# Optimization experiments

Measured on AMD Instinct MI355X. Metric: run time of the kernel, lower is better.

## Reference

```python
import jax, jax.numpy as jnp
import numpy as np

B, N, T = 32, 256, 256
W, H, EMB = 32, 128, 64          # window_size, tgcn_hidden_dim, gsl_embed_dim
K, ALPHA, NC, E = 3, 1.0, 16, 8192  # gsl_avg_steps, gsl_alpha, num_classes, static edges
GCN_IN = W + H                    # GSL gconv in_channels
THRESH = 1e-8


def setup_inputs():
    ks = jax.random.split(jax.random.key(0), 24)
    rng = np.random.default_rng(0)
    src = rng.integers(0, N, size=E)
    tgt = (src + 1 + rng.integers(0, N - 1, size=E)) % N  # no self-loops (PyG adds them)
    edge_index = jnp.asarray(np.stack([src, tgt]), dtype=jnp.int32)

    def p(k, shape):
        return jax.random.normal(k, shape, jnp.float32) * (shape[0] ** -0.5)

    z = lambda n: jnp.zeros((n,), jnp.float32)
    return {
        "x": jax.random.normal(ks[0], (B, N, T), jnp.float32),
        "static_edge_index": edge_index,
        "static_edge_weight": jax.random.uniform(ks[1], (E,), jnp.float32),
        "Wg": p(ks[2], (GCN_IN, EMB)), "bg": z(EMB),
        "W1": p(ks[3], (EMB, EMB)), "b1": z(EMB),
        "W2": p(ks[4], (EMB, EMB)), "b2": z(EMB),
        "Wz": p(ks[5], (W, H)), "bz": z(H),
        "Wr": p(ks[6], (W, H)), "br": z(H),
        "Wh": p(ks[7], (W, H)), "bh": z(H),
        "Wlz": p(ks[8], (2 * H, H)), "blz": z(H),
        "Wlr": p(ks[9], (2 * H, H)), "blr": z(H),
        "Wlh": p(ks[10], (2 * H, H)), "blh": z(H),
        "Wc": p(ks[11], (H * N, NC)), "bc": z(NC),
    }


def _forward(x, edge_index, edge_weight, Wg, bg, W1, b1, W2, b2,
             Wz, bz, Wr, br, Wh, bh, Wlz, blz, Wlr, blr, Wlh, blh, Wc, bc):
    dt = x.dtype
    eye = jnp.eye(N, dtype=dt)

    # Static graph: dense adjacency + self loops, symmetric GCN normalization.
    A = jnp.zeros((N, N), dt).at[edge_index[0], edge_index[1]].add(edge_weight) + eye
    deg = A.sum(0)  # in-degree at targets (col sums)
    di = jnp.where(deg > 0, jax.lax.rsqrt(deg), 0.0)
    S = di[:, None] * A * di[None, :]  # S[r,c]; out[c] = sum_r S[r,c] x[r]

    # windowing: v[t,b,n,:] = x[b,n,t*W:(t+1)*W]
    v = x.reshape(B, N, T // W, W).transpose(2, 0, 1, 3)  # [nw,B,N,W]

    def gcn_norm_b(Ad):  # Ad [B,N,N], zero diagonal guaranteed
        Ah = Ad + eye
        d = Ah.sum(-2)
        q = jnp.where(d > 0, jax.lax.rsqrt(d), 0.0)
        return q[:, :, None] * Ah * q[:, None, :]

    def step(carry, vt):
        h, hist, cnt = carry  # h [B,N,H], hist [K,B,N,N]
        It = jnp.concatenate([vt, h], -1)                   # [B,N,W+H]
        df = jnp.einsum('rc,brf->bcf', S, It @ Wg) + bg     # static GCNConv
        de1 = jnp.tanh(ALPHA * (df @ W1 + b1))
        de2 = jnp.tanh(ALPHA * (df @ W2 + b2))
        M = jnp.einsum('bne,bme->bnm', de1, de2)            # de1 @ de2^T
        Et = jax.nn.relu(jnp.tanh(ALPHA * (M - M.transpose(0, 2, 1))))
        hist = jnp.concatenate([hist[1:], Et[None]], 0)     # deque(maxlen=K)
        cnt = jnp.minimum(cnt + 1, K)
        Mt = hist.sum(0) / cnt.astype(dt)
        An = gcn_norm_b(jnp.where(Mt > THRESH, Mt, jnp.zeros((), dt)))

        def conv(Wk, bk):  # dynamic GCNConv, block-diag == per-batch dense
            return jnp.einsum('brc,brf->bcf', An, vt @ Wk) + bk

        Z = jax.nn.sigmoid(jnp.concatenate([conv(Wz, bz), h], -1) @ Wlz + blz)
        R = jax.nn.sigmoid(jnp.concatenate([conv(Wr, br), h], -1) @ Wlr + blr)
        Ht = jnp.tanh(jnp.concatenate([conv(Wh, bh), h * R], -1) @ Wlh + blh)
        h = Z * h + (1.0 - Z) * Ht
        return (h, hist, cnt), None

    h0 = jnp.zeros((B, N, H), dt)
    hist0 = jnp.zeros((K, B, N, N), dt)
    (h, _, _), _ = jax.lax.scan(step, (h0, hist0, jnp.int32(0)), v)
    return h.reshape(B, N * H) @ Wc + bc  # [B, NC]


def reference(x, static_edge_index, static_edge_weight, Wg, bg, W1, b1, W2, b2,
              Wz, bz, Wr, br, Wh, bh, Wlz, blz, Wlr, blr, Wlh, blh, Wc, bc):
    return _forward(x, static_edge_index, static_edge_weight, Wg, bg, W1, b1, W2, b2,
                    Wz, bz, Wr, br, Wh, bh, Wlz, blz, Wlr, blr, Wlh, blh, Wc, bc)
```

## Files before the change

kernel.cpp:

```cpp
#include <hip/hip_runtime.h>
#include <hip/hip_bf16.h>
#include <math.h>

#define BB  32
#define NN  256
#define TT  256
#define WW  32
#define HH  128
#define EMBD 64
#define NCLS 16
#define NE  8192

__device__ __forceinline__ float bf(const __hip_bfloat16* p, int i) {
    return __bfloat162float(p[i]);
}
__device__ __forceinline__ float ld3(const void* p, int i, int m) {
    if (m == 2) return (float)((const double*)p)[i];
    if (m == 1) return ((const float*)p)[i];
    return __bfloat162float(((const __hip_bfloat16*)p)[i]);
}
__device__ __forceinline__ float r16(float x) {
    return __bfloat162float(__float2bfloat16(x));
}
__device__ __forceinline__ float tanh_s(float x) {
    x = fminf(20.0f, fmaxf(-20.0f, x));
    return tanhf(x);
}
__device__ __forceinline__ float sig_s(float x) {
    x = fminf(30.0f, fmaxf(-30.0f, x));
    return 1.0f / (1.0f + expf(-x));
}


__global__ __launch_bounds__(64) void k_sentinel(float* out, float v) {
    int i = blockIdx.x * 64 + threadIdx.x;
    if (i < BB * NCLS) out[i] = v;
}

__global__ __launch_bounds__(256) void k_probe_all(
        const void* x, const void* ew, const void* Wg, const void* W1, const void* W2,
        const void* Wz, const void* Wr, const void* Wh, const void* Wlz, const void* Wlr,
        const void* Wlh, const void* Wc, int* insB, int* insF) {
    int sec = blockIdx.x >> 2, sub = blockIdx.x & 3;
    const void* p; int nB, idx;
    switch (sec) {
        case 0:  p = x;   nB = 32768; idx = 0;  break;
        case 1:  p = ew;  nB = 8192;  idx = 2;  break;
        case 2:  p = Wg;  nB = 10240; idx = 3;  break;
        case 3:  p = W1;  nB = 4096;  idx = 5;  break;
        case 4:  p = W2;  nB = 4096;  idx = 7;  break;
        case 5:  p = Wz;  nB = 4096;  idx = 9;  break;
        case 6:  p = Wr;  nB = 4096;  idx = 11; break;
        case 7:  p = Wh;  nB = 4096;  idx = 13; break;
        case 8:  p = Wlz; nB = 32768; idx = 15; break;
        case 9:  p = Wlr; nB = 32768; idx = 17; break;
        case 10: p = Wlh; nB = 32768; idx = 19; break;
        default: p = Wc;  nB = 32768; idx = 21; break;
    }
    int nF = nB >> 2;
    const __hip_bfloat16* pb = (const __hip_bfloat16*)p;
    const float* pf = (const float*)p;
    int start = sub * 256 + threadIdx.x;
    for (int i = start; i < nB; i += 1024) {
        float v = __bfloat162float(pb[i]);
        if (!(fabsf(v) < 64.0f)) { insB[idx] = 1; break; }
    }
    for (int i = start; i < nF; i += 1024) {
        float v = pf[i];
        if (!(fabsf(v) < 1e4f)) { insF[idx] = 1; break; }
    }
}

__global__ void k_resolve(const int* insB, const int* insF, int* modes) {
    int i = threadIdx.x;
    if (i < 32 && i != 1)
        modes[i] = insB[i] ? (insF[i] ? 2 : 1) : 0;
}

__global__ __launch_bounds__(64) void k_detect_ei(const int* ei, int* modes) {
    if (threadIdx.x == 0 && blockIdx.x == 0) {
        bool allz = true;
        for (int k = 1; k < 64; k += 2) if (ei[k] != 0) allz = false;
        modes[1] = allz ? 1 : 0;
    }
}

__global__ __launch_bounds__(256) void k_cvtall(const void* Wg, const void* W1, const void* W2,
                                                const void* Wz, const void* Wr, const void* Wh,
                                                const void* Wlz, const void* Wlr, const void* Wlh,
                                                const void* Wc, const int* modes, float* dst) {
    int i = blockIdx.x * 256 + threadIdx.x;
    if (i >= 665600) return;
    float v;
    if      (i < 10240)  v = ld3(Wg,  i,          modes[3]);
    else if (i < 14336)  v = ld3(W1,  i - 10240,  modes[5]);
    else if (i < 18432)  v = ld3(W2,  i - 14336,  modes[7]);
    else if (i < 22528)  v = ld3(Wz,  i - 18432,  modes[9]);
    else if (i < 26624)  v = ld3(Wr,  i - 22528,  modes[11]);
    else if (i < 30720)  v = ld3(Wh,  i - 26624,  modes[13]);
    else if (i < 63488)  v = ld3(Wlz, i - 30720,  modes[15]);
    else if (i < 96256)  v = ld3(Wlr, i - 63488,  modes[17]);
    else if (i < 129024) v = ld3(Wlh, i - 96256,  modes[19]);
    else if (i < 653312) v = ld3(Wc,  i - 129024, modes[21]);
    else {
        int j = i - 653312, w = j / 384, rem = j - w * 384;
        int g = rem >> 7, f = rem & 127;
        const void* Wk = (g == 0) ? Wz : ((g == 1) ? Wr : Wh);
        int mk = (g == 0) ? modes[9] : ((g == 1) ? modes[11] : modes[13]);
        v = ld3(Wk, w * 128 + f, mk);
    }
    dst[i] = v;
}

__global__ __launch_bounds__(256) void k_fuse(const float* Wzf, const float* Wrf, const float* Whf,
                                              const float* Wlzf, const float* Wlrf, const float* Wlhf,
                                              const __hip_bfloat16* bz, const __hip_bfloat16* br,
                                              const __hip_bfloat16* bh,
                                              const __hip_bfloat16* blz, const __hip_bfloat16* blr,
                                              const __hip_bfloat16* blh,
                                              float* Wf, float* bfv) {
    int g = blockIdx.y;
    const float* Wcv = (g == 0) ? Wzf : ((g == 1) ? Wrf : Whf);
    const float* Wl  = (g == 0) ? Wlzf : ((g == 1) ? Wlrf : Wlhf);
    const __hip_bfloat16* bcv = (g == 0) ? bz : ((g == 1) ? br : bh);
    const __hip_bfloat16* blv = (g == 0) ? blz : ((g == 1) ? blr : blh);
    int idx = blockIdx.x * 256 + threadIdx.x;
    if (idx >= 160 * 128) return;
    int k = idx >> 7, f = idx & 127;
    float v;
    if (k < 32) {
        float acc = 0.f;
        for (int m = 0; m < 128; m++) acc += Wcv[k * 128 + m] * Wl[m * 128 + f];
        v = acc;
    } else {
        v = Wl[(k + 96) * 128 + f];
    }
    Wf[((size_t)g * 160 + k) * 128 + f] = v;
    if (idx < 128) {
        float acc = __bfloat162float(blv[idx]);
        for (int m = 0; m < 128; m++) acc += __bfloat162float(bcv[m]) * Wl[m * 128 + idx];
        bfv[g * 128 + idx] = acc;
    }
}


__global__ __launch_bounds__(256) void k_scatter(const int* ei, const void* ew, float* A,
                                                 const int* modes) {
    int e = blockIdx.x * 256 + threadIdx.x;
    if (e < NE) {
        int s, t;
        if (modes[1]) { s = ei[2 * e]; t = ei[2 * (NE + e)]; }
        else          { s = ei[e];     t = ei[NE + e]; }
        float w = r16(ld3(ew, e, modes[2]));
        if ((unsigned)s < NN && (unsigned)t < NN)
            atomicAdd(&A[s * NN + t], w);
    }
    if (blockIdx.x == 0) atomicAdd(&A[threadIdx.x * NN + threadIdx.x], 1.0f);
}

__global__ __launch_bounds__(256) void k_roundA(float* A) {
    int i = blockIdx.x * 256 + threadIdx.x;
    A[i] = r16(A[i]);
}

__global__ __launch_bounds__(256) void k_di(const float* A, float* di) {
    int wave = threadIdx.x >> 6, lane = threadIdx.x & 63;
    int c = blockIdx.x * 4 + wave;
    float s = 0.f;
    for (int r = lane; r < NN; r += 64) s += A[r * NN + c];
    for (int o = 32; o > 0; o >>= 1) s += __shfl_down(s, o, 64);
    if (lane == 0) {
        float deg = r16(s);
        di[c] = (deg > 0.f) ? r16(1.0f / sqrtf(deg)) : 0.0f;
    }
}

__global__ __launch_bounds__(256) void k_St(const float* A, const float* di, float* St) {
    int idx = blockIdx.x * 256 + threadIdx.x;
    int c = idx >> 8, r = idx & 255;
    St[idx] = r16(r16(di[r] * A[r * NN + c]) * di[c]);
}


__global__ __launch_bounds__(256) void k1_itwg4(const void* x, const float* h,
                                                const float* Wgf, float* Y,
                                                int t, const int* modes) {
    __shared__ float vt[4][32];
    __shared__ float hr[4][128];
    int b = blockIdx.y, n0 = blockIdx.x * 4;
    int tid = threadIdx.x;
    int nd = tid >> 6, f = tid & 63;
    if (f < WW) vt[nd][f] = ld3(x, (b * NN + n0 + nd) * TT + t * WW + f, modes[0]);
    size_t hb = (size_t)(b * NN + n0 + nd) * HH;
    hr[nd][f] = h[hb + f];
    hr[nd][f + 64] = h[hb + f + 64];
    __syncthreads();
    float acc = 0.f;
    for (int k = 0; k < WW; k++)  acc += vt[nd][k] * Wgf[k * EMBD + f];
    for (int k = 0; k < HH; k++)  acc += hr[nd][k] * Wgf[(WW + k) * EMBD + f];
    if (t == 0 && modes[0] == 0 && modes[3] == 0) acc = r16(acc);
    Y[(size_t)(b * NN + n0 + nd) * EMBD + f] = acc;
}

__global__ __launch_bounds__(256) void k23g(const float* St, const float* Y,
                                            const __hip_bfloat16* bg,
                                            const float* W1f, const float* W2f,
                                            const __hip_bfloat16* b1, const __hip_bfloat16* b2,
                                            float* de1, float* de2, float* qsum,
                                            int t, const int* modes) {
    __shared__ float As[32][36];
    __shared__ float Bs[32][68];
    __shared__ float dfT[64][36];
    int b = blockIdx.y, c0 = blockIdx.x * 32;
    int tid = threadIdx.x;
    if (blockIdx.x == 0) qsum[b * NN + tid] = 0.f;
    int tm = tid >> 4, tn = tid & 15;
    int am = tid & 31, ak0 = (tid >> 5) * 4;
    int bk = tid >> 3, bn0 = (tid & 7) * 8;
    const float* Yb = Y + (size_t)b * (NN * EMBD);
    float acc[2][4] = {};
    for (int kb = 0; kb < 256; kb += 32) {
        float4 a0 = *(const float4*)(St + (size_t)(c0 + am) * 256 + kb + ak0);
        float av4[4] = {a0.x, a0.y, a0.z, a0.w};
        int rot = (tid >> 5) & 3;
#pragma unroll
        for (int jj = 0; jj < 4; jj++) { int j = (jj + rot) & 3; As[ak0 + j][am] = av4[j]; }
        const float* bp = Yb + (size_t)(kb + bk) * 64 + bn0;
        *(float4*)&Bs[bk][bn0]     = *(const float4*)bp;
        *(float4*)&Bs[bk][bn0 + 4] = *(const float4*)(bp + 4);
        __syncthreads();
#pragma unroll
        for (int kk = 0; kk < 32; kk++) {
            float2 av = *(const float2*)&As[kk][tm * 2];
            float4 bv = *(const float4*)&Bs[kk][tn * 4];
            float aa[2] = {av.x, av.y};
            float bb[4] = {bv.x, bv.y, bv.z, bv.w};
#pragma unroll
            for (int i = 0; i < 2; i++)
#pragma unroll
                for (int j = 0; j < 4; j++) acc[i][j] += aa[i] * bb[j];
        }
        __syncthreads();
    }
    bool rnd = (t == 0 && modes[0] == 0 && modes[3] == 0);
#pragma unroll
    for (int i = 0; i < 2; i++)
#pragma unroll
        for (int j = 0; j < 4; j++) {
            int f = tn * 4 + j;
            float v = (rnd ? r16(acc[i][j]) : acc[i][j]) + bf(bg, f);
            dfT[f][tm * 2 + i] = v;
        }
    __syncthreads();
    float a1acc[2][4] = {};
    for (int kb2 = 0; kb2 < 64; kb2 += 32) {
        const float* bp = W1f + (size_t)(kb2 + bk) * 64 + bn0;
        *(float4*)&Bs[bk][bn0]     = *(const float4*)bp;
        *(float4*)&Bs[bk][bn0 + 4] = *(const float4*)(bp + 4);
        __syncthreads();
#pragma unroll
        for (int kk = 0; kk < 32; kk++) {
            float2 av = *(const float2*)&dfT[kb2 + kk][tm * 2];
            float4 bv = *(const float4*)&Bs[kk][tn * 4];
            float aa[2] = {av.x, av.y};
            float bb[4] = {bv.x, bv.y, bv.z, bv.w};
#pragma unroll
            for (int i = 0; i < 2; i++)
#pragma unroll
                for (int j = 0; j < 4; j++) a1acc[i][j] += aa[i] * bb[j];
        }
        __syncthreads();
    }
#pragma unroll
    for (int i = 0; i < 2; i++) {
        int row = b * NN + c0 + tm * 2 + i;
        float4 o;
        o.x = tanh_s(a1acc[i][0] + bf(b1, tn * 4 + 0));
        o.y = tanh_s(a1acc[i][1] + bf(b1, tn * 4 + 1));
        o.z = tanh_s(a1acc[i][2] + bf(b1, tn * 4 + 2));
        o.w = tanh_s(a1acc[i][3] + bf(b1, tn * 4 + 3));
        *(float4*)&de1[(size_t)row * 64 + tn * 4] = o;
    }
    float a2acc[2][4] = {};
    for (int kb2 = 0; kb2 < 64; kb2 += 32) {
        const float* bp = W2f + (size_t)(kb2 + bk) * 64 + bn0;
        *(float4*)&Bs[bk][bn0]     = *(const float4*)bp;
        *(float4*)&Bs[bk][bn0 + 4] = *(const float4*)(bp + 4);
        __syncthreads();
#pragma unroll
        for (int kk = 0; kk < 32; kk++) {
            float2 av = *(const float2*)&dfT[kb2 + kk][tm * 2];
            float4 bv = *(const float4*)&Bs[kk][tn * 4];
            float aa[2] = {av.x, av.y};
            float bb[4] = {bv.x, bv.y, bv.z, bv.w};
#pragma unroll
            for (int i = 0; i < 2; i++)
#pragma unroll
                for (int j = 0; j < 4; j++) a2acc[i][j] += aa[i] * bb[j];
        }
        __syncthreads();
    }
#pragma unroll
    for (int i = 0; i < 2; i++) {
        int row = b * NN + c0 + tm * 2 + i;
        float4 o;
        o.x = tanh_s(a2acc[i][0] + bf(b2, tn * 4 + 0));
        o.y = tanh_s(a2acc[i][1] + bf(b2, tn * 4 + 1));
        o.z = tanh_s(a2acc[i][2] + bf(b2, tn * 4 + 2));
        o.w = tanh_s(a2acc[i][3] + bf(b2, tn * 4 + 3));
        *(float4*)&de2[(size_t)row * 64 + tn * 4] = o;
    }
}

__global__ __launch_bounds__(256) void k45(const float* de1, const float* de2,
                                           float* hist, float* AhT, float* qsum,
                                           int slabW, int slabR, float inv_cnt) {
    __shared__ float As[32][68];
    __shared__ float Bs[32][68];
    __shared__ float m2b[64][65];
    __shared__ float qpart[64];
    int b = blockIdx.z, r0 = blockIdx.x * 64, c0 = blockIdx.y * 64;
    int tid = threadIdx.x;
    if (tid < 64) qpart[tid] = 0.f;
    int tn = tid & 15, tm = tid >> 4;
    int am = tid >> 2, ak0 = (tid & 3) * 8;
    int rot = (tid & 3) * 2;
    const float* d1 = de1 + (size_t)b * (NN * EMBD);
    const float* d2 = de2 + (size_t)b * (NN * EMBD);
    float acc2[4][4] = {};
    for (int kb = 0; kb < 64; kb += 32) {
        const float* ap = d1 + (size_t)(c0 + am) * 64 + kb + ak0;
        float4 a0 = *(const float4*)ap;
        float4 a1 = *(const float4*)(ap + 4);
        float av8[8] = {a0.x, a0.y, a0.z, a0.w, a1.x, a1.y, a1.z, a1.w};
#pragma unroll
        for (int jj = 0; jj < 8; jj++) { int j = (jj + rot) & 7; As[ak0 + j][am] = av8[j]; }
        const float* bp = d2 + (size_t)(r0 + am) * 64 + kb + ak0;
        float4 b0 = *(const float4*)bp;
        float4 b1v = *(const float4*)(bp + 4);
        float bv8[8] = {b0.x, b0.y, b0.z, b0.w, b1v.x, b1v.y, b1v.z, b1v.w};
#pragma unroll
        for (int jj = 0; jj < 8; jj++) { int j = (jj + rot) & 7; Bs[ak0 + j][am] = bv8[j]; }
        __syncthreads();
#pragma unroll
        for (int kk = 0; kk < 32; kk++) {
            float4 av = *(const float4*)&As[kk][tm * 4];
            float4 bv = *(const float4*)&Bs[kk][tn * 4];
            float aa[4] = {av.x, av.y, av.z, av.w};
            float bb[4] = {bv.x, bv.y, bv.z, bv.w};
#pragma unroll
            for (int i = 0; i < 4; i++)
#pragma unroll
                for (int j = 0; j < 4; j++) acc2[i][j] += aa[i] * bb[j];
        }
        __syncthreads();
    }
#pragma unroll
    for (int i = 0; i < 4; i++)
#pragma unroll
        for (int j = 0; j < 4; j++) m2b[tm * 4 + i][tn * 4 + j] = acc2[i][j];
    float acc1[4][4] = {};
    for (int kb = 0; kb < 64; kb += 32) {
        const float* ap = d1 + (size_t)(r0 + am) * 64 + kb + ak0;
        float4 a0 = *(const float4*)ap;
        float4 a1 = *(const float4*)(ap + 4);
        float av8[8] = {a0.x, a0.y, a0.z, a0.w, a1.x, a1.y, a1.z, a1.w};
#pragma unroll
        for (int jj = 0; jj < 8; jj++) { int j = (jj + rot) & 7; As[ak0 + j][am] = av8[j]; }
        const float* bp = d2 + (size_t)(c0 + am) * 64 + kb + ak0;
        float4 b0 = *(const float4*)bp;
        float4 b1v = *(const float4*)(bp + 4);
        float bv8[8] = {b0.x, b0.y, b0.z, b0.w, b1v.x, b1v.y, b1v.z, b1v.w};
#pragma unroll
        for (int jj = 0; jj < 8; jj++) { int j = (jj + rot) & 7; Bs[ak0 + j][am] = bv8[j]; }
        __syncthreads();
#pragma unroll
        for (int kk = 0; kk < 32; kk++) {
            float4 av = *(const float4*)&As[kk][tm * 4];
            float4 bv = *(const float4*)&Bs[kk][tn * 4];
            float aa[4] = {av.x, av.y, av.z, av.w};
            float bb[4] = {bv.x, bv.y, bv.z, bv.w};
#pragma unroll
            for (int i = 0; i < 4; i++)
#pragma unroll
                for (int j = 0; j < 4; j++) acc1[i][j] += aa[i] * bb[j];
        }
        __syncthreads();
    }
    size_t NB = (size_t)BB * NN * NN;
    float* hsW = hist + (size_t)slabW * NB;
    const float* hsR = hist + (size_t)slabR * NB;
    float ad[4][4];
#pragma unroll
    for (int i = 0; i < 4; i++) {
        int r = r0 + tm * 4 + i;
        size_t o = ((size_t)(b * NN + r)) * NN + c0 + tn * 4;
        float4 e2v = *(const float4*)&hsW[o];
        float4 e1v = *(const float4*)&hsR[o];
        float e2a[4] = {e2v.x, e2v.y, e2v.z, e2v.w};
        float e1a[4] = {e1v.x, e1v.y, e1v.z, e1v.w};
        float4 ew4;
        float eo[4];
#pragma unroll
        for (int j = 0; j < 4; j++) {
            int c = c0 + tn * 4 + j;
            float e = tanh_s(acc1[i][j] - m2b[tn * 4 + j][tm * 4 + i]);
            e = e > 0.f ? e : 0.f;
            eo[j] = e;
            float mt = (e + e1a[j] + e2a[j]) * inv_cnt;
            float adv = (mt > 1e-8f) ? mt : 0.f;
            if (r == c) adv += 1.f;
            ad[i][j] = adv;
        }
        ew4.x = eo[0]; ew4.y = eo[1]; ew4.z = eo[2]; ew4.w = eo[3];
        *(float4*)&hsW[o] = ew4;
    }
#pragma unroll
    for (int j = 0; j < 4; j++) {
        float cs = ad[0][j] + ad[1][j] + ad[2][j] + ad[3][j];
        atomicAdd(&qpart[tn * 4 + j], cs);
    }
    __syncthreads();
#pragma unroll
    for (int i = 0; i < 4; i++)
#pragma unroll
        for (int j = 0; j < 4; j++) m2b[tn * 4 + j][tm * 4 + i] = ad[i][j];
    __syncthreads();
#pragma unroll
    for (int kk = 0; kk < 4; kk++) {
        int e = tid + kk * 256;
        int cl = e >> 4, q4 = e & 15;
        float4 o;
        o.x = m2b[cl][q4 * 4 + 0]; o.y = m2b[cl][q4 * 4 + 1];
        o.z = m2b[cl][q4 * 4 + 2]; o.w = m2b[cl][q4 * 4 + 3];
        *(float4*)&AhT[((size_t)(b * NN + c0 + cl)) * NN + r0 + q4 * 4] = o;
    }
    if (tid < 64) atomicAdd(&qsum[b * NN + c0 + tid], qpart[tid]);
}

__global__ __launch_bounds__(256) void k8a(const float* AhT, const void* x, const float* qsum,
                                           float* G, int t, const int* modes) {
    __shared__ float As[32][36];
    __shared__ float Bs[32][36];
    int b = blockIdx.y, c0 = blockIdx.x * 32;
    int tid = threadIdx.x;
    int tm = tid >> 3, tn = tid & 7;
    int am = tid & 31, ak0 = (tid >> 5) * 8;
    int rB = tid >> 3, w0 = (tid & 7) * 4;
    int m0 = modes[0];
    const float* Ab = AhT + (size_t)b * (NN * NN);
    float acc[4] = {0, 0, 0, 0};
    for (int kb = 0; kb < 256; kb += 32) {
        const float* ap = Ab + (size_t)(c0 + am) * 256 + kb + ak0;
        float4 a0 = *(const float4*)ap;
        float4 a1 = *(const float4*)(ap + 4);
        float av8[8] = {a0.x, a0.y, a0.z, a0.w, a1.x, a1.y, a1.z, a1.w};
#pragma unroll
        for (int j = 0; j < 8; j++) As[ak0 + j][am] = av8[j];
        int r = kb + rB;
        float qr = 1.0f / sqrtf(fmaxf(qsum[b * NN + r], 1e-12f));
        int xbase = (b * NN + r) * TT + t * WW + w0;
        float pv[4];
#pragma unroll
        for (int i = 0; i < 4; i++) pv[i] = qr * ld3(x, xbase + i, m0);
        int rot = rB & 3;
#pragma unroll
        for (int i = 0; i < 4; i++) {
            int j = (i + rot) & 3;
            Bs[rB][w0 + j] = pv[j];
        }
        __syncthreads();
#pragma unroll
        for (int kk = 0; kk < 32; kk++) {
            float a = As[kk][tm];
            float4 bv = *(const float4*)&Bs[kk][tn * 4];
            acc[0] += a * bv.x; acc[1] += a * bv.y;
            acc[2] += a * bv.z; acc[3] += a * bv.w;
        }
        __syncthreads();
    }
    int c = c0 + tm;
    float qc = 1.0f / sqrtf(fmaxf(qsum[b * NN + c], 1e-12f));
    float4 o = make_float4(qc * acc[0], qc * acc[1], qc * acc[2], qc * acc[3]);
    *(float4*)&G[((size_t)(b * NN + c)) * 32 + tn * 4] = o;
}

__global__ __launch_bounds__(256) void kZRH16(const float* G, float* h,
                                              const float* Wf, const float* bfv,
                                              const float* Wgf, const void* x, float* Y,
                                              int t, const int* modes) {
    __shared__ float As[160 * 18];
    __shared__ float Bs[2 * 32 * 128];
    int r0 = blockIdx.x * 16;
    int tid = threadIdx.x;
    int m0 = modes[0];
    if (tid < 128) {
        int r = tid >> 3, c4 = (tid & 7) * 4;
        float4 gv = *(const float4*)&G[(size_t)(r0 + r) * 32 + c4];
        As[(c4 + 0) * 18 + r] = gv.x;
        As[(c4 + 1) * 18 + r] = gv.y;
        As[(c4 + 2) * 18 + r] = gv.z;
        As[(c4 + 3) * 18 + r] = gv.w;
    }
#pragma unroll
    for (int u = 0; u < 2; u++) {
        int e = tid * 2 + u;
        int r = e >> 5, c4 = (e & 31) * 4;
        float4 hv = *(const float4*)&h[(size_t)(r0 + r) * 128 + c4];
        As[(32 + c4 + 0) * 18 + r] = hv.x;
        As[(32 + c4 + 1) * 18 + r] = hv.y;
        As[(32 + c4 + 2) * 18 + r] = hv.z;
        As[(32 + c4 + 3) * 18 + r] = hv.w;
    }
    int rg = tid >> 5, cg = tid & 31;
    float zv[2][4], rv[2][4];
    {
        const float* W0 = Wf;
        const float* W1 = Wf + (size_t)(160 * 128);
        float accZ[2][4] = {};
        float accR[2][4] = {};
        for (int kb = 0; kb < 160; kb += 32) {
#pragma unroll
            for (int u = 0; u < 4; u++) {
                int e = tid + u * 256;
                int kk = e >> 5, c4 = (e & 31) * 4;
                *(float4*)&Bs[kk * 128 + c4]        = *(const float4*)&W0[(size_t)(kb + kk) * 128 + c4];
                *(float4*)&Bs[4096 + kk * 128 + c4] = *(const float4*)&W1[(size_t)(kb + kk) * 128 + c4];
            }
            __syncthreads();
#pragma unroll 4
            for (int kk = 0; kk < 32; kk++) {
                float2 av = *(const float2*)&As[(kb + kk) * 18 + rg * 2];
                float4 b0 = *(const float4*)&Bs[kk * 128 + cg * 4];
                float4 b1 = *(const float4*)&Bs[4096 + kk * 128 + cg * 4];
                accZ[0][0] += av.x * b0.x; accZ[0][1] += av.x * b0.y;
                accZ[0][2] += av.x * b0.z; accZ[0][3] += av.x * b0.w;
                accZ[1][0] += av.y * b0.x; accZ[1][1] += av.y * b0.y;
                accZ[1][2] += av.y * b0.z; accZ[1][3] += av.y * b0.w;
                accR[0][0] += av.x * b1.x; accR[0][1] += av.x * b1.y;
                accR[0][2] += av.x * b1.z; accR[0][3] += av.x * b1.w;
                accR[1][0] += av.y * b1.x; accR[1][1] += av.y * b1.y;
                accR[1][2] += av.y * b1.z; accR[1][3] += av.y * b1.w;
            }
            __syncthreads();
        }
#pragma unroll
        for (int i = 0; i < 2; i++)
#pragma unroll
            for (int j = 0; j < 4; j++) {
                zv[i][j] = sig_s(accZ[i][j] + bfv[cg * 4 + j]);
                rv[i][j] = sig_s(accR[i][j] + bfv[128 + cg * 4 + j]);
            }
    }
#pragma unroll
    for (int i = 0; i < 2; i++)
#pragma unroll
        for (int j = 0; j < 4; j++) {
            int slot = (32 + cg * 4 + j) * 18 + rg * 2 + i;
            As[slot] = As[slot] * rv[i][j];
        }
    __syncthreads();
    float acc[2][4] = {};
    {
        const float* Wgp = Wf + (size_t)2 * (160 * 128);
        for (int kb = 0; kb < 160; kb += 32) {
#pragma unroll
            for (int u = 0; u < 4; u++) {
                int e = tid + u * 256;
                int kk = e >> 5, c4 = (e & 31) * 4;
                *(float4*)&Bs[kk * 128 + c4] = *(const float4*)&Wgp[(size_t)(kb + kk) * 128 + c4];
            }
            __syncthreads();
#pragma unroll 4
            for (int kk = 0; kk < 32; kk++) {
                float2 av = *(const float2*)&As[(kb + kk) * 18 + rg * 2];
                float4 bv = *(const float4*)&Bs[kk * 128 + cg * 4];
                acc[0][0] += av.x * bv.x; acc[0][1] += av.x * bv.y;
                acc[0][2] += av.x * bv.z; acc[0][3] += av.x * bv.w;
                acc[1][0] += av.y * bv.x; acc[1][1] += av.y * bv.y;
                acc[1][2] += av.y * bv.z; acc[1][3] += av.y * bv.w;
            }
            __syncthreads();
        }
    }
#pragma unroll
    for (int i = 0; i < 2; i++) {
        int row = r0 + rg * 2 + i;
        size_t o = (size_t)row * 128 + cg * 4;
        float4 hv = *(const float4*)&h[o];
        float4 r;
        r.x = zv[i][0] * hv.x + (1.0f - zv[i][0]) * tanh_s(acc[i][0] + bfv[256 + cg * 4 + 0]);
        r.y = zv[i][1] * hv.y + (1.0f - zv[i][1]) * tanh_s(acc[i][1] + bfv[256 + cg * 4 + 1]);
        r.z = zv[i][2] * hv.z + (1.0f - zv[i][2]) * tanh_s(acc[i][2] + bfv[256 + cg * 4 + 2]);
        r.w = zv[i][3] * hv.w + (1.0f - zv[i][3]) * tanh_s(acc[i][3] + bfv[256 + cg * 4 + 3]);
        *(float4*)&h[o] = r;
        As[(32 + cg * 4 + 0) * 18 + rg * 2 + i] = r.x;
        As[(32 + cg * 4 + 1) * 18 + rg * 2 + i] = r.y;
        As[(32 + cg * 4 + 2) * 18 + rg * 2 + i] = r.z;
        As[(32 + cg * 4 + 3) * 18 + rg * 2 + i] = r.w;
    }
    if (t < 7) {
#pragma unroll
        for (int u = 0; u < 2; u++) {
            int e = tid * 2 + u;
            int r = e >> 5, w = e & 31;
            As[w * 18 + r] = ld3(x, (r0 + r) * TT + (t + 1) * WW + w, m0);
        }
        __syncthreads();
        int yr = tid >> 4, yc4 = (tid & 15) * 4;
        float yacc[4] = {0.f, 0.f, 0.f, 0.f};
        for (int kb = 0; kb < 160; kb += 32) {
#pragma unroll
            for (int u = 0; u < 2; u++) {
                int e = tid * 2 + u;
                int kk = e >> 4, c4 = (e & 15) * 4;
                *(float4*)&Bs[kk * 64 + c4] = *(const float4*)&Wgf[(size_t)(kb + kk) * 64 + c4];
            }
            __syncthreads();
#pragma unroll 4
            for (int kk = 0; kk < 32; kk++) {
                float a = As[(kb + kk) * 18 + yr];
                float4 bv = *(const float4*)&Bs[kk * 64 + yc4];
                yacc[0] += a * bv.x; yacc[1] += a * bv.y;
                yacc[2] += a * bv.z; yacc[3] += a * bv.w;
            }
            __syncthreads();
        }
        *(float4*)&Y[(size_t)(r0 + yr) * 64 + yc4] =
            make_float4(yacc[0], yacc[1], yacc[2], yacc[3]);
    }
}

__global__ __launch_bounds__(256) void k10a(const float* h, const float* Wcf, float* partial) {
    __shared__ float red[16][17];
    int chunk = blockIdx.x, b = blockIdx.y;
    int c = threadIdx.x & 15, isub = threadIdx.x >> 4;
    const float* hb = h + (size_t)b * (NN * HH);
    int i0 = chunk * 2048;
    float acc = 0.f;
    for (int s = 0; s < 128; s++) {
        int i = i0 + isub + 16 * s;
        acc += hb[i] * Wcf[(size_t)i * NCLS + c];
    }
    red[isub][c] = acc;
    __syncthreads();
    for (int st = 8; st > 0; st >>= 1) {
        if (isub < st) red[isub][c] += red[isub + st][c];
        __syncthreads();
    }
    if (isub == 0) partial[((size_t)(b * NCLS + c)) * 16 + chunk] = red[0][c];
}

__global__ __launch_bounds__(512) void k10b(const float* partial, const __hip_bfloat16* bcb,
                                            float* out) {
    int tid = threadIdx.x;
    if (tid < BB * NCLS) {
        int c = tid & 15;
        float s = 0.f;
        for (int k = 0; k < 16; k++) s += partial[(size_t)tid * 16 + k];
        out[tid] = s + bf(bcb, c);
    }
}


extern "C" void kernel_launch(void* const* d_in, const int* in_sizes, int n_in,
                              void* d_out, int out_size, void* d_ws, size_t ws_size,
                              hipStream_t stream) {
    float* out = (float*)d_out;

    static const int exp_sizes[23] = {2097152, 16384, 8192, 10240, 64, 4096, 64, 4096, 64,
                                      4096, 128, 4096, 128, 4096, 128, 32768, 128, 32768, 128,
                                      32768, 128, 524288, 16};
    if (n_in != 23) { k_sentinel<<<8, 64, 0, stream>>>(out, 4444.0f); return; }
    for (int i = 0; i < 23; i++) {
        if (in_sizes[i] != exp_sizes[i]) {
            k_sentinel<<<8, 64, 0, stream>>>(out, (float)(4000 + i));
            return;
        }
    }

    const void* x   = d_in[0];
    const int*  ei  = (const int*)d_in[1];
    const void* ew  = d_in[2];
    const void* Wg  = d_in[3];
    const __hip_bfloat16* bg  = (const __hip_bfloat16*)d_in[4];
    const void* W1  = d_in[5];
    const __hip_bfloat16* b1  = (const __hip_bfloat16*)d_in[6];
    const void* W2  = d_in[7];
    const __hip_bfloat16* b2  = (const __hip_bfloat16*)d_in[8];
    const void* Wz  = d_in[9];
    const __hip_bfloat16* bz  = (const __hip_bfloat16*)d_in[10];
    const void* Wr  = d_in[11];
    const __hip_bfloat16* br  = (const __hip_bfloat16*)d_in[12];
    const void* Wh  = d_in[13];
    const __hip_bfloat16* bh  = (const __hip_bfloat16*)d_in[14];
    const void* Wlz = d_in[15];
    const __hip_bfloat16* blz = (const __hip_bfloat16*)d_in[16];
    const void* Wlr = d_in[17];
    const __hip_bfloat16* blr = (const __hip_bfloat16*)d_in[18];
    const void* Wlh = d_in[19];
    const __hip_bfloat16* blh = (const __hip_bfloat16*)d_in[20];
    const void* Wc  = d_in[21];
    const __hip_bfloat16* bcb = (const __hip_bfloat16*)d_in[22];

    float* ws = (float*)d_ws;
    const size_t off_A    = 0;
    const size_t off_hist = off_A + 65536;
    const size_t off_h    = off_hist + 2u * 2097152;
    const size_t off_flag = off_h + 1048576;
    const size_t off_mode = off_flag + 16;
    const size_t off_insB = off_mode + 32;
    const size_t off_insF = off_insB + 32;
    const size_t zero_end = off_insF + 32;
    const size_t off_St   = zero_end;
    const size_t off_di   = off_St + 65536;
    const size_t off_q    = off_di + 256;
    const size_t off_AhT  = off_q + 8192;
    const size_t off_Yp   = off_AhT + 2097152;
    const size_t off_C    = off_Yp + 3145728;
    const size_t off_wts  = off_C + 3145728;
    const size_t need_bytes = (off_wts + 665600u) * sizeof(float);

    if (ws_size < need_bytes) {
        k_sentinel<<<8, 64, 0, stream>>>(out, (float)ws_size);
        return;
    }

    float* A    = ws + off_A;
    float* hist = ws + off_hist;
    float* h    = ws + off_h;
    int*   modes= (int*)(ws + off_mode);
    int*   insB = (int*)(ws + off_insB);
    int*   insF = (int*)(ws + off_insF);
    float* St   = ws + off_St;
    float* di   = ws + off_di;
    float* qsum = ws + off_q;
    float* AhT  = ws + off_AhT;
    float* wts  = ws + off_wts;
    float* Y    = ws + off_Yp;
    float* de1  = ws + off_Yp + 1048576;
    float* de2  = ws + off_Yp + 1572864;
    float* G    = ws + off_Yp + 2097152;
    float* Wf   = ws + off_C;
    float* bfv  = ws + off_C + 61440;
    float* partial = qsum;

    float* Wgf  = wts;
    float* W1f  = wts + 10240;
    float* W2f  = wts + 14336;
    float* Wzf  = wts + 18432;
    float* Wrf  = wts + 22528;
    float* Whf  = wts + 26624;
    float* Wlzf = wts + 30720;
    float* Wlrf = wts + 63488;
    float* Wlhf = wts + 96256;
    float* Wcf  = wts + 129024;

    hipMemsetAsync(ws, 0, zero_end * sizeof(float), stream);

    k_probe_all<<<48, 256, 0, stream>>>(x, ew, Wg, W1, W2, Wz, Wr, Wh, Wlz, Wlr, Wlh, Wc,
                                        insB, insF);
    k_resolve<<<1, 32, 0, stream>>>(insB, insF, modes);
    k_detect_ei<<<1, 64, 0, stream>>>(ei, modes);
    k_cvtall<<<2600, 256, 0, stream>>>(Wg, W1, W2, Wz, Wr, Wh, Wlz, Wlr, Wlh, Wc, modes, wts);
    k_fuse<<<dim3(80, 3), 256, 0, stream>>>(Wzf, Wrf, Whf, Wlzf, Wlrf, Wlhf,
                                            bz, br, bh, blz, blr, blh, Wf, bfv);

    k_scatter<<<NE / 256, 256, 0, stream>>>(ei, ew, A, modes);
    k_roundA<<<NN * NN / 256, 256, 0, stream>>>(A);
    k_di<<<NN / 4, 256, 0, stream>>>(A, di);
    k_St<<<NN * NN / 256, 256, 0, stream>>>(A, di, St);

    for (int t = 0; t < 8; t++) {
        if (t == 0)
            k1_itwg4<<<dim3(NN / 4, BB), 256, 0, stream>>>(x, h, Wgf, Y, 0, modes);
        k23g<<<dim3(8, BB), 256, 0, stream>>>(St, Y, bg, W1f, W2f, b1, b2,
                                              de1, de2, qsum, t, modes);
        float inv_cnt = 1.0f / (float)((t + 1 < 3) ? (t + 1) : 3);
        k45<<<dim3(4, 4, BB), 256, 0, stream>>>(de1, de2, hist, AhT, qsum,
                                                t & 1, (t + 1) & 1, inv_cnt);
        k8a<<<dim3(NN / 32, BB), 256, 0, stream>>>(AhT, x, qsum, G, t, modes);
        kZRH16<<<NN * BB / 16, 256, 0, stream>>>(G, h, Wf, bfv, Wgf, x, Y, t, modes);
    }

    k10a<<<dim3(16, BB), 256, 0, stream>>>(h, Wcf, partial);
    k10b<<<1, 512, 0, stream>>>(partial, bcb, out);
}
```

Before: 874.2 us.

## Fuse normalized adjacency-times-window GEMM into the ZRH gate kernel

Removes the separate k8a kernel that computed G = q_c * AhT * (q_r * x_window) and instead computes each 16-row block of G inside kZRH16, writing it straight into the shared-memory A tile. This drops one launch per timestep and the global round-trip through the G buffer. In exchange, each of the 512 blocks reloads the full 256x32 normalized window slice for its batch (16x redundant x reads) and runs a scalar inner product loop, and shared memory use grows.

```diff
diff --git a/kernel.cpp b/kernel.cpp
--- a/kernel.cpp
+++ b/kernel.cpp
@@ -438,70 +438,17 @@
     if (tid < 64) atomicAdd(&qsum[b * NN + c0 + tid], qpart[tid]);
 }
 
-__global__ __launch_bounds__(256) void k8a(const float* AhT, const void* x, const float* qsum,
-                                           float* G, int t, const int* modes) {
-    __shared__ float As[32][36];
-    __shared__ float Bs[32][36];
-    int b = blockIdx.y, c0 = blockIdx.x * 32;
-    int tid = threadIdx.x;
-    int tm = tid >> 3, tn = tid & 7;
-    int am = tid & 31, ak0 = (tid >> 5) * 8;
-    int rB = tid >> 3, w0 = (tid & 7) * 4;
-    int m0 = modes[0];
-    const float* Ab = AhT + (size_t)b * (NN * NN);
-    float acc[4] = {0, 0, 0, 0};
-    for (int kb = 0; kb < 256; kb += 32) {
-        const float* ap = Ab + (size_t)(c0 + am) * 256 + kb + ak0;
-        float4 a0 = *(const float4*)ap;
-        float4 a1 = *(const float4*)(ap + 4);
-        float av8[8] = {a0.x, a0.y, a0.z, a0.w, a1.x, a1.y, a1.z, a1.w};
-#pragma unroll
-        for (int j = 0; j < 8; j++) As[ak0 + j][am] = av8[j];
-        int r = kb + rB;
-        float qr = 1.0f / sqrtf(fmaxf(qsum[b * NN + r], 1e-12f));
-        int xbase = (b * NN + r) * TT + t * WW + w0;
-        float pv[4];
-#pragma unroll
-        for (int i = 0; i < 4; i++) pv[i] = qr * ld3(x, xbase + i, m0);
-        int rot = rB & 3;
-#pragma unroll
-        for (int i = 0; i < 4; i++) {
-            int j = (i + rot) & 3;
-            Bs[rB][w0 + j] = pv[j];
-        }
-        __syncthreads();
-#pragma unroll
-        for (int kk = 0; kk < 32; kk++) {
-            float a = As[kk][tm];
-            float4 bv = *(const float4*)&Bs[kk][tn * 4];
-            acc[0] += a * bv.x; acc[1] += a * bv.y;
-            acc[2] += a * bv.z; acc[3] += a * bv.w;
-        }
-        __syncthreads();
-    }
-    int c = c0 + tm;
-    float qc = 1.0f / sqrtf(fmaxf(qsum[b * NN + c], 1e-12f));
-    float4 o = make_float4(qc * acc[0], qc * acc[1], qc * acc[2], qc * acc[3]);
-    *(float4*)&G[((size_t)(b * NN + c)) * 32 + tn * 4] = o;
-}
-
-__global__ __launch_bounds__(256) void kZRH16(const float* G, float* h,
+__global__ __launch_bounds__(256) void kZRH16(const float* AhT, const float* qsum, float* h,
                                               const float* Wf, const float* bfv,
                                               const float* Wgf, const void* x, float* Y,
                                               int t, const int* modes) {
+    __shared__ float qrow[256];
     __shared__ float As[160 * 18];
-    __shared__ float Bs[2 * 32 * 128];
+    __shared__ float Bs[8448];
     int r0 = blockIdx.x * 16;
+    int b  = r0 >> 8;
     int tid = threadIdx.x;
     int m0 = modes[0];
-    if (tid < 128) {
-        int r = tid >> 3, c4 = (tid & 7) * 4;
-        float4 gv = *(const float4*)&G[(size_t)(r0 + r) * 32 + c4];
-        As[(c4 + 0) * 18 + r] = gv.x;
-        As[(c4 + 1) * 18 + r] = gv.y;
-        As[(c4 + 2) * 18 + r] = gv.z;
-        As[(c4 + 3) * 18 + r] = gv.w;
-    }
 #pragma unroll
     for (int u = 0; u < 2; u++) {
         int e = tid * 2 + u;
@@ -512,6 +459,42 @@
         As[(32 + c4 + 2) * 18 + r] = hv.z;
         As[(32 + c4 + 3) * 18 + r] = hv.w;
     }
+    qrow[tid] = 1.0f / sqrtf(fmaxf(qsum[b * NN + tid], 1e-12f));
+    __syncthreads();
+
+    {
+        float* vtq = Bs;
+        float* Ah  = Bs + 4096;
+        float gacc[2] = {0.f, 0.f};
+        int gi = tid & 15, gw = (tid >> 4) * 2;
+        for (int half = 0; half < 2; half++) {
+            int wv = tid & 31, rb = tid >> 5;
+#pragma unroll
+            for (int k = 0; k < 16; k++) {
+                int rl = rb + 8 * k;
+                int rg = half * 128 + rl;
+                vtq[rl * 32 + wv] = qrow[rg] * ld3(x, (b * NN + rg) * TT + t * WW + wv, m0);
+            }
+            {
+                int i = tid >> 4, c8 = (tid & 15) * 8;
+                const float* ap = AhT + (size_t)(r0 + i) * NN + half * 128 + c8;
+                *(float4*)&Ah[i * 132 + c8]     = *(const float4*)ap;
+                *(float4*)&Ah[i * 132 + c8 + 4] = *(const float4*)(ap + 4);
+            }
+            __syncthreads();
+            for (int r = 0; r < 128; r++) {
+                float a = Ah[gi * 132 + r];
+                float2 v = *(const float2*)&vtq[r * 32 + gw];
+                gacc[0] += a * v.x;
+                gacc[1] += a * v.y;
+            }
+            __syncthreads();
+        }
+        float qc = qrow[(r0 & 255) + gi];
+        As[gw * 18 + gi]       = qc * gacc[0];
+        As[(gw + 1) * 18 + gi] = qc * gacc[1];
+    }
+
     int rg = tid >> 5, cg = tid & 31;
     float zv[2][4], rv[2][4];
     {
@@ -740,7 +723,6 @@
     float* Y    = ws + off_Yp;
     float* de1  = ws + off_Yp + 1048576;
     float* de2  = ws + off_Yp + 1572864;
-    float* G    = ws + off_Yp + 2097152;
     float* Wf   = ws + off_C;
     float* bfv  = ws + off_C + 61440;
     float* partial = qsum;
@@ -779,8 +761,7 @@
         float inv_cnt = 1.0f / (float)((t + 1 < 3) ? (t + 1) : 3);
         k45<<<dim3(4, 4, BB), 256, 0, stream>>>(de1, de2, hist, AhT, qsum,
                                                 t & 1, (t + 1) & 1, inv_cnt);
-        k8a<<<dim3(NN / 32, BB), 256, 0, stream>>>(AhT, x, qsum, G, t, modes);
-        kZRH16<<<NN * BB / 16, 256, 0, stream>>>(G, h, Wf, bfv, Wgf, x, Y, t, modes);
+        kZRH16<<<NN * BB / 16, 256, 0, stream>>>(AhT, qsum, h, Wf, bfv, Wgf, x, Y, t, modes);
     }
 
     k10a<<<dim3(16, BB), 256, 0, stream>>>(h, Wcf, partial);
```

Result: no change. 869.6 us (-0.5%).
